# Kernel optimization log

Hardware: AMD Instinct MI355X
Metric: run time of the kernel (lower is better)

Reference implementation:

```python
import jax, jax.numpy as jnp
import numpy as np

# ---- static hyperparams (from comp_encoding.__init__ / DMPNNEncoderLayer) ----
B = 512            # number of molecules in the batch (wrapper's python loop)
A = 128            # padded atoms per molecule == max_mol_len
E = 256            # padded directed bonds per molecule
K = 6              # max incoming bonds gathered per bond/atom
ATOM_FDIM = 133
BOND_FDIM = 14
H = 128            # d_hidden = max_mol_len
DEPTH = 3
G = 2048           # global feature dim (Morgan fingerprint)


def _mol_lens():
    ml = np.array(jax.random.randint(jax.random.fold_in(jax.random.key(0), 5), (B,), 16, H + 1))
    ml[0] = H  # ensure comp_dim == max(mol_lens) == H so per-row padding is a no-op
    return ml


def setup_inputs() -> dict:
    key = jax.random.key(0)
    ks = jax.random.split(key, 10)
    atom_feature = jax.random.normal(ks[0], (B, A, ATOM_FDIM), jnp.float32)
    f_ini_atoms_bond = jax.random.normal(ks[1], (B, E, ATOM_FDIM + BOND_FDIM), jnp.float32)
    atom_to_incoming_bond = jax.random.randint(ks[2], (B, A, K), 0, E)
    mapping = jax.random.randint(ks[3], (B, E, K), 0, E)
    global_f = jax.random.normal(ks[4], (B, G), jnp.float32)
    mol_lens = _mol_lens()  # static numpy ints (constants, drive output shapes)
    W_i = jax.random.normal(ks[6], (H, ATOM_FDIM + BOND_FDIM), jnp.float32) / np.float32(np.sqrt(ATOM_FDIM + BOND_FDIM))
    W_h = jax.random.normal(ks[7], (H, H), jnp.float32) / np.float32(np.sqrt(H))
    W_o = jax.random.normal(ks[8], (H, ATOM_FDIM + H), jnp.float32) / np.float32(np.sqrt(ATOM_FDIM + H))
    b_o = jax.random.normal(ks[9], (H,), jnp.float32) * 0.01
    return dict(atom_feature=atom_feature, f_ini_atoms_bond=f_ini_atoms_bond,
                atom_to_incoming_bond=atom_to_incoming_bond, mapping=mapping,
                global_f=global_f, mol_lens=mol_lens,
                W_i=W_i, W_h=W_h, W_o=W_o, b_o=b_o)


def _gather_sum(msg, idx):
    # msg: [B, E, H]; idx: [B, N, K] -> sum over K incoming messages: [B, N, H]
    b, n, k = idx.shape
    g = jnp.take_along_axis(msg, idx.reshape(b, n * k)[..., None], axis=1)
    return g.reshape(b, n, k, -1).sum(axis=2)


def reference(atom_feature, f_ini_atoms_bond, atom_to_incoming_bond, mapping,
              global_f, mol_lens, W_i, W_h, W_o, b_o):
    # DMPNN: W_i on initial directed-bond features
    inp = jnp.einsum('bef,hf->beh', f_ini_atoms_bond, W_i)   # [B, E, H]
    msg = jax.nn.relu(inp)
    for _ in range(DEPTH - 1):
        agg = _gather_sum(msg, mapping)                      # [B, E, H]
        msg = jax.nn.relu(inp + jnp.einsum('beh,gh->beg', agg, W_h))
    m2a = _gather_sum(msg, atom_to_incoming_bond)            # [B, A, H]
    cat = jnp.concatenate([atom_feature, m2a], axis=-1)      # [B, A, 133+H]
    atoms_h = jax.nn.relu(jnp.einsum('bad,hd->bah', cat, W_o) + b_o)  # [B, A, H]

    # wrapper: take first mol_len atom encodings per molecule, stack, build mask
    ml = np.asarray(mol_lens)
    valid = np.arange(A)[None, :] < ml[:, None]              # [B, A] static
    b_idx, a_idx = np.nonzero(valid)
    comp = atoms_h[b_idx, a_idx]                             # [sum(mol_lens), H]
    c_mask = jnp.asarray(valid.astype(np.float32))           # [B, comp_dim]
    return comp, c_mask
```

## Files before the change

### kernel.cpp

```cpp
#include <hip/hip_runtime.h>
#include <hip/hip_bf16.h>

typedef unsigned int   uint;
typedef unsigned short ushort;
typedef short bf16x8 __attribute__((ext_vector_type(8)));
typedef float f32x4  __attribute__((ext_vector_type(4)));

constexpr int Bm   = 512;
constexpr int Aa   = 128;
constexpr int Ee   = 256;
constexpr int Kk   = 6;
constexpr int AFD  = 133;
constexpr int FD   = 147;
constexpr int Hh   = 128;
constexpr int CATD = 261;
constexpr int KWI  = 192;
constexpr int KWO  = 320;
constexpr int MST  = 136;

__device__ __forceinline__ ushort f2b(float f) {
    uint u = __float_as_uint(f);
    u += 0x7FFFu + ((u >> 16) & 1u);
    return (ushort)(u >> 16);
}
__device__ __forceinline__ uint cvt2(float x, float y) {
    float2 t2; t2.x = x; t2.y = y;
    __hip_bfloat162 t = __float22bfloat162_rn(t2);
    uint r; __builtin_memcpy(&r, &t, 4); return r;
}
__device__ __forceinline__ float2 b2f2(uint p) {
    float2 r;
    r.x = __uint_as_float(p << 16);
    r.y = __uint_as_float(p & 0xFFFF0000u);
    return r;
}

__device__ __forceinline__ bf16x8 gsum6(const ushort* src, const int* mr, int ko) {
    float2 s0 = {0.f, 0.f}, s1 = {0.f, 0.f}, s2 = {0.f, 0.f}, s3 = {0.f, 0.f};
#pragma unroll
    for (int k = 0; k < Kk; ++k) {
        uint4 m = *(const uint4*)&src[mr[k] + ko];
        float2 a = b2f2(m.x); s0.x += a.x; s0.y += a.y;
        float2 b = b2f2(m.y); s1.x += b.x; s1.y += b.y;
        float2 d = b2f2(m.z); s2.x += d.x; s2.y += d.y;
        float2 e = b2f2(m.w); s3.x += e.x; s3.y += e.y;
    }
    uint4 o;
    o.x = cvt2(s0.x, s0.y); o.y = cvt2(s1.x, s1.y);
    o.z = cvt2(s2.x, s2.y); o.w = cvt2(s3.x, s3.y);
    bf16x8 r;
    __builtin_memcpy(&r, &o, 16);
    return r;
}

__device__ __forceinline__ bf16x8 ld_frag_f32(const float* sp, int c0, int lim) {
    float v[8];
#pragma unroll
    for (int d = 0; d < 8; ++d) v[d] = (c0 + d < lim) ? sp[d] : 0.f;
    uint4 o;
    o.x = cvt2(v[0], v[1]); o.y = cvt2(v[2], v[3]);
    o.z = cvt2(v[4], v[5]); o.w = cvt2(v[6], v[7]);
    bf16x8 r;
    __builtin_memcpy(&r, &o, 16);
    return r;
}

__global__ __launch_bounds__(256) void k_prep_w(const float* __restrict__ Wi,
                                                const float* __restrict__ Wh,
                                                const float* __restrict__ Wo,
                                                ushort* __restrict__ Wi_b,
                                                ushort* __restrict__ Wh_b,
                                                ushort* __restrict__ Wo_b) {
    const int h = blockIdx.x, t = threadIdx.x;
    for (int c = t; c < KWI; c += 256)
        Wi_b[h * KWI + c] = f2b(c < FD ? Wi[h * FD + c] : 0.f);
    for (int c = t; c < Hh; c += 256)
        Wh_b[h * Hh + c] = f2b(Wh[h * Hh + c]);
    for (int c = t; c < KWO; c += 256) {
        float v = 0.f;
        if (c < AFD)       v = Wo[h * CATD + c];
        else if (c >= 192) v = Wo[h * CATD + AFD + (c - 192)];
        Wo_b[h * KWO + c] = f2b(v);
    }
}

__global__ __launch_bounds__(512) void k_scan(const int* __restrict__ ml,
                                              int* __restrict__ pfx) {
    __shared__ int s[512];
    int t = threadIdx.x;
    s[t] = ml[t];
    __syncthreads();
    for (int off = 1; off < 512; off <<= 1) {
        int v = (t >= off) ? s[t - off] : 0;
        __syncthreads();
        s[t] += v;
        __syncthreads();
    }
    pfx[t + 1] = s[t];
    if (t == 0) pfx[0] = 0;
}

__global__ __launch_bounds__(512, 2) void k_fused(
        const float* __restrict__ atomf,
        const float* __restrict__ fini,
        const int*   __restrict__ a2ib,
        const int*   __restrict__ mapping,
        const ushort* __restrict__ Wi_b,
        const ushort* __restrict__ Wh_b,
        const ushort* __restrict__ Wo_b,
        const float* __restrict__ bo,
        const int*   __restrict__ mol_lens,
        const int*   __restrict__ pfx,
        float* __restrict__ out,
        float* __restrict__ cmask) {
    __shared__ ushort msg[Ee * MST];
    __shared__ int    map_s[Ee * Kk];
    __shared__ int    a2_s[Aa * Kk];

    const int b    = blockIdx.x;
    const int tid  = threadIdx.x;
    const int wave = tid >> 6;
    const int lane = tid & 63;
    const int l15  = lane & 15, quad = lane >> 4;

    for (int i = tid; i < Ee * Kk; i += 512) map_s[i] = mapping[b * Ee * Kk + i];
    for (int i = tid; i < Aa * Kk; i += 512) a2_s[i]  = a2ib[b * Aa * Kk + i];
    const int len = mol_lens[b];
    if (tid < Aa) cmask[b * Aa + tid] = (tid < len) ? 1.0f : 0.0f;

    f32x4 acc[2][8];
#pragma unroll
    for (int i = 0; i < 2; ++i)
#pragma unroll
        for (int j = 0; j < 8; ++j) acc[i][j] = (f32x4){0.f, 0.f, 0.f, 0.f};

    const float* fsrc = fini + (size_t)b * Ee * FD;
#pragma unroll
    for (int c = 0; c < 3; ++c) {
#pragma unroll
        for (int ks = 0; ks < 2; ++ks) {
            const int c0 = c * 64 + ks * 32 + quad * 8;
            bf16x8 af[2];
#pragma unroll
            for (int i = 0; i < 2; ++i) {
                const int row = wave * 32 + i * 16 + l15;
                af[i] = ld_frag_f32(fsrc + (size_t)row * FD + c0, c0, FD);
            }
#pragma unroll
            for (int jh = 0; jh < 2; ++jh) {
                bf16x8 bf[4];
#pragma unroll
                for (int j = 0; j < 4; ++j)
                    bf[j] = *(const bf16x8*)&Wi_b[((jh * 4 + j) * 16 + l15) * KWI + c0];
#pragma unroll
                for (int i = 0; i < 2; ++i)
#pragma unroll
                    for (int j = 0; j < 4; ++j)
                        acc[i][jh * 4 + j] = __builtin_amdgcn_mfma_f32_16x16x32_bf16(
                            af[i], bf[j], acc[i][jh * 4 + j], 0, 0, 0);
            }
        }
    }

    uint2 inp_pk[2][8];
#pragma unroll
    for (int i = 0; i < 2; ++i)
#pragma unroll
        for (int j = 0; j < 8; ++j) {
            f32x4 a4 = acc[i][j];
            uint2 p;
            p.x = cvt2(a4[0], a4[1]);
            p.y = cvt2(a4[2], a4[3]);
            inp_pk[i][j] = p;
            int col = j * 16 + l15;
#pragma unroll
            for (int reg = 0; reg < 4; ++reg) {
                int row = wave * 32 + i * 16 + quad * 4 + reg;
                float v = a4[reg] > 0.f ? a4[reg] : 0.f;
                msg[row * MST + col] = f2b(v);
            }
        }
    __syncthreads();

    int mr[2][Kk];
#pragma unroll
    for (int i = 0; i < 2; ++i) {
        int row = wave * 32 + i * 16 + l15;
#pragma unroll
        for (int k = 0; k < Kk; ++k) mr[i][k] = map_s[row * Kk + k] * MST;
    }

#pragma unroll
    for (int h = 0; h < 2; ++h) {
#pragma unroll
        for (int i = 0; i < 2; ++i)
#pragma unroll
            for (int j = 0; j < 8; ++j) {
                float2 lo = b2f2(inp_pk[i][j].x);
                float2 hi = b2f2(inp_pk[i][j].y);
                acc[i][j] = (f32x4){lo.x, lo.y, hi.x, hi.y};
            }
#pragma unroll
        for (int ks = 0; ks < 4; ++ks) {
            const int ko = ks * 32 + quad * 8;
            bf16x8 af[2];
#pragma unroll
            for (int i = 0; i < 2; ++i) af[i] = gsum6(msg, mr[i], ko);
#pragma unroll
            for (int jh = 0; jh < 2; ++jh) {
                bf16x8 bf[4];
#pragma unroll
                for (int j = 0; j < 4; ++j)
                    bf[j] = *(const bf16x8*)&Wh_b[((jh * 4 + j) * 16 + l15) * Hh + ko];
#pragma unroll
                for (int i = 0; i < 2; ++i)
#pragma unroll
                    for (int j = 0; j < 4; ++j)
                        acc[i][jh * 4 + j] = __builtin_amdgcn_mfma_f32_16x16x32_bf16(
                            af[i], bf[j], acc[i][jh * 4 + j], 0, 0, 0);
            }
        }
        __syncthreads();
#pragma unroll
        for (int i = 0; i < 2; ++i)
#pragma unroll
            for (int j = 0; j < 8; ++j) {
                int col = j * 16 + l15;
#pragma unroll
                for (int reg = 0; reg < 4; ++reg) {
                    int row = wave * 32 + i * 16 + quad * 4 + reg;
                    float v = acc[i][j][reg];
                    msg[row * MST + col] = f2b(v > 0.f ? v : 0.f);
                }
            }
        __syncthreads();
    }

    f32x4 ro[8];
#pragma unroll
    for (int j = 0; j < 8; ++j) ro[j] = (f32x4){0.f, 0.f, 0.f, 0.f};

    {
        int ar[Kk];
        const int row = wave * 16 + l15;
#pragma unroll
        for (int k = 0; k < Kk; ++k) ar[k] = a2_s[row * Kk + k] * MST;
#pragma unroll
        for (int ks = 0; ks < 4; ++ks) {
            const int ko = ks * 32 + quad * 8;
            bf16x8 a0 = gsum6(msg, ar, ko);
#pragma unroll
            for (int jh = 0; jh < 2; ++jh) {
                bf16x8 bf[4];
#pragma unroll
                for (int j = 0; j < 4; ++j)
                    bf[j] = *(const bf16x8*)&Wo_b[((jh * 4 + j) * 16 + l15) * KWO + 192 + ko];
#pragma unroll
                for (int j = 0; j < 4; ++j)
                    ro[jh * 4 + j] = __builtin_amdgcn_mfma_f32_16x16x32_bf16(
                        a0, bf[j], ro[jh * 4 + j], 0, 0, 0);
            }
        }
    }

    const float* asrc = atomf + (size_t)b * Aa * AFD;
#pragma unroll
    for (int c = 0; c < 3; ++c) {
#pragma unroll
        for (int ks = 0; ks < 2; ++ks) {
            const int c0 = c * 64 + ks * 32 + quad * 8;
            const int row = wave * 16 + l15;
            bf16x8 a0 = ld_frag_f32(asrc + (size_t)row * AFD + c0, c0, AFD);
#pragma unroll
            for (int jh = 0; jh < 2; ++jh) {
                bf16x8 bf[4];
#pragma unroll
                for (int j = 0; j < 4; ++j)
                    bf[j] = *(const bf16x8*)&Wo_b[((jh * 4 + j) * 16 + l15) * KWO + c0];
#pragma unroll
                for (int j = 0; j < 4; ++j)
                    ro[jh * 4 + j] = __builtin_amdgcn_mfma_f32_16x16x32_bf16(
                        a0, bf[j], ro[jh * 4 + j], 0, 0, 0);
            }
        }
    }

    const int base = pfx[b];
#pragma unroll
    for (int j = 0; j < 8; ++j) {
        int col = j * 16 + l15;
        float bv = bo[col];
#pragma unroll
        for (int reg = 0; reg < 4; ++reg) {
            int a = wave * 16 + quad * 4 + reg;
            if (a < len) {
                float v = ro[j][reg] + bv;
                out[(size_t)(base + a) * Hh + col] = v > 0.f ? v : 0.f;
            }
        }
    }
}

extern "C" void kernel_launch(void* const* d_in, const int* in_sizes, int n_in,
                              void* d_out, int out_size, void* d_ws, size_t ws_size,
                              hipStream_t stream) {
    const float* atom_feature = (const float*)d_in[0];
    const float* f_ini        = (const float*)d_in[1];
    const int*   a2ib         = (const int*)d_in[2];
    const int*   mapping      = (const int*)d_in[3];
    const int*   mol_lens     = (const int*)d_in[5];
    const float* Wi           = (const float*)d_in[6];
    const float* Wh           = (const float*)d_in[7];
    const float* Wo           = (const float*)d_in[8];
    const float* bo           = (const float*)d_in[9];
    float* out = (float*)d_out;

    ushort* Wi_b = (ushort*)d_ws;
    ushort* Wh_b = Wi_b + 128 * KWI;
    ushort* Wo_b = Wh_b + 128 * Hh;
    int*    pfx  = (int*)(Wo_b + 128 * KWO);

    float* cmask = out + ((size_t)out_size - (size_t)Bm * Aa);

    k_prep_w<<<128, 256, 0, stream>>>(Wi, Wh, Wo, Wi_b, Wh_b, Wo_b);
    k_scan  <<<1, 512, 0, stream>>>(mol_lens, pfx);
    k_fused <<<Bm, 512, 0, stream>>>(atom_feature, f_ini, a2ib, mapping,
                                     Wi_b, Wh_b, Wo_b, bo, mol_lens, pfx,
                                     out, cmask);
}
```

Measured before the change: 274.6 us.

## Swizzle message LDS layout and load gather indices straight into registers

Replaces the padded message tile in shared memory (row stride 136) with an unpadded 128-wide layout that XOR-swizzles 8-element column groups by row, so both the scattered stores and the 16-byte gathers avoid bank conflicts. The mapping and atom-to-bond index tables no longer go through shared memory; each lane reads its own six indices from global memory into registers. This shrinks LDS use per block, which may allow more resident blocks, and drops a staging pass and a barrier dependency. The cost is extra XOR arithmetic on every message access and uncoalesced global index loads.

```diff
diff --git a/kernel.cpp b/kernel.cpp
--- a/kernel.cpp
+++ b/kernel.cpp
@@ -16,7 +16,10 @@
 constexpr int CATD = 261;
 constexpr int KWI  = 192;
 constexpr int KWO  = 320;
-constexpr int MST  = 136;
+
+__device__ __forceinline__ int msg_idx(int row, int col) {
+    return row * 128 + (col ^ ((row & 7) << 3));
+}
 
 __device__ __forceinline__ ushort f2b(float f) {
     uint u = __float_as_uint(f);
@@ -39,7 +42,8 @@
     float2 s0 = {0.f, 0.f}, s1 = {0.f, 0.f}, s2 = {0.f, 0.f}, s3 = {0.f, 0.f};
 #pragma unroll
     for (int k = 0; k < Kk; ++k) {
-        uint4 m = *(const uint4*)&src[mr[k] + ko];
+        const int sw = (mr[k] >> 4) & 56;
+        uint4 m = *(const uint4*)&src[mr[k] + (ko ^ sw)];
         float2 a = b2f2(m.x); s0.x += a.x; s0.y += a.y;
         float2 b = b2f2(m.y); s1.x += b.x; s1.y += b.y;
         float2 d = b2f2(m.z); s2.x += d.x; s2.y += d.y;
@@ -113,9 +117,7 @@
         const int*   __restrict__ pfx,
         float* __restrict__ out,
         float* __restrict__ cmask) {
-    __shared__ ushort msg[Ee * MST];
-    __shared__ int    map_s[Ee * Kk];
-    __shared__ int    a2_s[Aa * Kk];
+    __shared__ ushort msg[Ee * 128];
 
     const int b    = blockIdx.x;
     const int tid  = threadIdx.x;
@@ -123,10 +125,17 @@
     const int lane = tid & 63;
     const int l15  = lane & 15, quad = lane >> 4;
 
-    for (int i = tid; i < Ee * Kk; i += 512) map_s[i] = mapping[b * Ee * Kk + i];
-    for (int i = tid; i < Aa * Kk; i += 512) a2_s[i]  = a2ib[b * Aa * Kk + i];
     const int len = mol_lens[b];
     if (tid < Aa) cmask[b * Aa + tid] = (tid < len) ? 1.0f : 0.0f;
+
+    int mr[2][Kk];
+#pragma unroll
+    for (int i = 0; i < 2; ++i) {
+        const int row = wave * 32 + i * 16 + l15;
+        const int* mp = &mapping[((size_t)b * Ee + row) * Kk];
+#pragma unroll
+        for (int k = 0; k < Kk; ++k) mr[i][k] = mp[k] * 128;
+    }
 
     f32x4 acc[2][8];
 #pragma unroll
@@ -172,23 +181,15 @@
             p.x = cvt2(a4[0], a4[1]);
             p.y = cvt2(a4[2], a4[3]);
             inp_pk[i][j] = p;
-            int col = j * 16 + l15;
+            const int col = j * 16 + l15;
 #pragma unroll
             for (int reg = 0; reg < 4; ++reg) {
-                int row = wave * 32 + i * 16 + quad * 4 + reg;
+                const int row = wave * 32 + i * 16 + quad * 4 + reg;
                 float v = a4[reg] > 0.f ? a4[reg] : 0.f;
-                msg[row * MST + col] = f2b(v);
+                msg[msg_idx(row, col)] = f2b(v);
             }
         }
     __syncthreads();
-
-    int mr[2][Kk];
-#pragma unroll
-    for (int i = 0; i < 2; ++i) {
-        int row = wave * 32 + i * 16 + l15;
-#pragma unroll
-        for (int k = 0; k < Kk; ++k) mr[i][k] = map_s[row * Kk + k] * MST;
-    }
 
 #pragma unroll
     for (int h = 0; h < 2; ++h) {
@@ -225,12 +226,12 @@
         for (int i = 0; i < 2; ++i)
 #pragma unroll
             for (int j = 0; j < 8; ++j) {
-                int col = j * 16 + l15;
+                const int col = j * 16 + l15;
 #pragma unroll
                 for (int reg = 0; reg < 4; ++reg) {
-                    int row = wave * 32 + i * 16 + quad * 4 + reg;
+                    const int row = wave * 32 + i * 16 + quad * 4 + reg;
                     float v = acc[i][j][reg];
-                    msg[row * MST + col] = f2b(v > 0.f ? v : 0.f);
+                    msg[msg_idx(row, col)] = f2b(v > 0.f ? v : 0.f);
                 }
             }
         __syncthreads();
@@ -239,12 +240,14 @@
     f32x4 ro[8];
 #pragma unroll
     for (int j = 0; j < 8; ++j) ro[j] = (f32x4){0.f, 0.f, 0.f, 0.f};
+
+    const int arow = wave * 16 + l15;
 
     {
         int ar[Kk];
-        const int row = wave * 16 + l15;
-#pragma unroll
-        for (int k = 0; k < Kk; ++k) ar[k] = a2_s[row * Kk + k] * MST;
+        const int* ap = &a2ib[((size_t)b * Aa + arow) * Kk];
+#pragma unroll
+        for (int k = 0; k < Kk; ++k) ar[k] = ap[k] * 128;
 #pragma unroll
         for (int ks = 0; ks < 4; ++ks) {
             const int ko = ks * 32 + quad * 8;
@@ -269,8 +272,7 @@
 #pragma unroll
         for (int ks = 0; ks < 2; ++ks) {
             const int c0 = c * 64 + ks * 32 + quad * 8;
-            const int row = wave * 16 + l15;
-            bf16x8 a0 = ld_frag_f32(asrc + (size_t)row * AFD + c0, c0, AFD);
+            bf16x8 a0 = ld_frag_f32(asrc + (size_t)arow * AFD + c0, c0, AFD);
 #pragma unroll
             for (int jh = 0; jh < 2; ++jh) {
                 bf16x8 bf[4];
@@ -288,11 +290,11 @@
     const int base = pfx[b];
 #pragma unroll
     for (int j = 0; j < 8; ++j) {
-        int col = j * 16 + l15;
-        float bv = bo[col];
+        const int col = j * 16 + l15;
+        const float bv = bo[col];
 #pragma unroll
         for (int reg = 0; reg < 4; ++reg) {
-            int a = wave * 16 + quad * 4 + reg;
+            const int a = wave * 16 + quad * 4 + reg;
             if (a < len) {
                 float v = ro[j][reg] + bv;
                 out[(size_t)(base + a) * Hh + col] = v > 0.f ? v : 0.f;
```

Result: slower. 297.4 us (+8.3%).

## Stage bond and atom features into LDS as bf16 before MFMA GEMMs

Applied to the files above, without the earlier changes.

The kernel now copies each molecule's fp32 bond-feature and atom-feature rows into a padded bf16 shared-memory buffer with coalesced loads. Previously each lane did strided 8-float global reads and converted them per fragment. The atom-feature staging is placed inside the second message-passing iteration so its loads can overlap compute, and the K loop shrinks from 192 to 160 columns. The new ~78KB staging buffer roughly doubles LDS use per block, which likely drops residency from two blocks per CU to one.

```diff
diff --git a/kernel.cpp b/kernel.cpp
--- a/kernel.cpp
+++ b/kernel.cpp
@@ -17,6 +17,7 @@
 constexpr int KWI  = 192;
 constexpr int KWO  = 320;
 constexpr int MST  = 136;
+constexpr int FST  = 152;
 
 __device__ __forceinline__ ushort f2b(float f) {
     uint u = __float_as_uint(f);
@@ -48,18 +49,6 @@
     uint4 o;
     o.x = cvt2(s0.x, s0.y); o.y = cvt2(s1.x, s1.y);
     o.z = cvt2(s2.x, s2.y); o.w = cvt2(s3.x, s3.y);
-    bf16x8 r;
-    __builtin_memcpy(&r, &o, 16);
-    return r;
-}
-
-__device__ __forceinline__ bf16x8 ld_frag_f32(const float* sp, int c0, int lim) {
-    float v[8];
-#pragma unroll
-    for (int d = 0; d < 8; ++d) v[d] = (c0 + d < lim) ? sp[d] : 0.f;
-    uint4 o;
-    o.x = cvt2(v[0], v[1]); o.y = cvt2(v[2], v[3]);
-    o.z = cvt2(v[4], v[5]); o.w = cvt2(v[6], v[7]);
     bf16x8 r;
     __builtin_memcpy(&r, &o, 16);
     return r;
@@ -113,6 +102,7 @@
         const int*   __restrict__ pfx,
         float* __restrict__ out,
         float* __restrict__ cmask) {
+    __shared__ ushort stage_l[Ee * FST + 8];
     __shared__ ushort msg[Ee * MST];
     __shared__ int    map_s[Ee * Kk];
     __shared__ int    a2_s[Aa * Kk];
@@ -123,10 +113,19 @@
     const int lane = tid & 63;
     const int l15  = lane & 15, quad = lane >> 4;
 
+    const float* fsrc = fini + (size_t)b * Ee * FD;
+    for (int i = tid; i < Ee * FST; i += 512) {
+        int r = i / FST;
+        int c = i - r * FST;
+        float v = (c < FD) ? fsrc[r * FD + c] : 0.f;
+        stage_l[i] = f2b(v);
+    }
+    if (tid < 8) stage_l[Ee * FST + tid] = 0;
     for (int i = tid; i < Ee * Kk; i += 512) map_s[i] = mapping[b * Ee * Kk + i];
     for (int i = tid; i < Aa * Kk; i += 512) a2_s[i]  = a2ib[b * Aa * Kk + i];
     const int len = mol_lens[b];
     if (tid < Aa) cmask[b * Aa + tid] = (tid < len) ? 1.0f : 0.0f;
+    __syncthreads();
 
     f32x4 acc[2][8];
 #pragma unroll
@@ -134,31 +133,27 @@
 #pragma unroll
         for (int j = 0; j < 8; ++j) acc[i][j] = (f32x4){0.f, 0.f, 0.f, 0.f};
 
-    const float* fsrc = fini + (size_t)b * Ee * FD;
-#pragma unroll
-    for (int c = 0; c < 3; ++c) {
-#pragma unroll
-        for (int ks = 0; ks < 2; ++ks) {
-            const int c0 = c * 64 + ks * 32 + quad * 8;
-            bf16x8 af[2];
-#pragma unroll
-            for (int i = 0; i < 2; ++i) {
-                const int row = wave * 32 + i * 16 + l15;
-                af[i] = ld_frag_f32(fsrc + (size_t)row * FD + c0, c0, FD);
-            }
-#pragma unroll
-            for (int jh = 0; jh < 2; ++jh) {
-                bf16x8 bf[4];
+#pragma unroll
+    for (int ksi = 0; ksi < 5; ++ksi) {
+        const int c0 = ksi * 32 + quad * 8;
+        bf16x8 af[2];
+#pragma unroll
+        for (int i = 0; i < 2; ++i) {
+            const int row = wave * 32 + i * 16 + l15;
+            af[i] = *(const bf16x8*)&stage_l[row * FST + c0];
+        }
+#pragma unroll
+        for (int jh = 0; jh < 2; ++jh) {
+            bf16x8 bf[4];
+#pragma unroll
+            for (int j = 0; j < 4; ++j)
+                bf[j] = *(const bf16x8*)&Wi_b[((jh * 4 + j) * 16 + l15) * KWI + c0];
+#pragma unroll
+            for (int i = 0; i < 2; ++i)
 #pragma unroll
                 for (int j = 0; j < 4; ++j)
-                    bf[j] = *(const bf16x8*)&Wi_b[((jh * 4 + j) * 16 + l15) * KWI + c0];
-#pragma unroll
-                for (int i = 0; i < 2; ++i)
-#pragma unroll
-                    for (int j = 0; j < 4; ++j)
-                        acc[i][jh * 4 + j] = __builtin_amdgcn_mfma_f32_16x16x32_bf16(
-                            af[i], bf[j], acc[i][jh * 4 + j], 0, 0, 0);
-            }
+                    acc[i][jh * 4 + j] = __builtin_amdgcn_mfma_f32_16x16x32_bf16(
+                        af[i], bf[j], acc[i][jh * 4 + j], 0, 0, 0);
         }
     }
 
@@ -172,10 +167,10 @@
             p.x = cvt2(a4[0], a4[1]);
             p.y = cvt2(a4[2], a4[3]);
             inp_pk[i][j] = p;
-            int col = j * 16 + l15;
+            const int col = j * 16 + l15;
 #pragma unroll
             for (int reg = 0; reg < 4; ++reg) {
-                int row = wave * 32 + i * 16 + quad * 4 + reg;
+                const int row = wave * 32 + i * 16 + quad * 4 + reg;
                 float v = a4[reg] > 0.f ? a4[reg] : 0.f;
                 msg[row * MST + col] = f2b(v);
             }
@@ -185,13 +180,22 @@
     int mr[2][Kk];
 #pragma unroll
     for (int i = 0; i < 2; ++i) {
-        int row = wave * 32 + i * 16 + l15;
+        const int row = wave * 32 + i * 16 + l15;
 #pragma unroll
         for (int k = 0; k < Kk; ++k) mr[i][k] = map_s[row * Kk + k] * MST;
     }
 
 #pragma unroll
     for (int h = 0; h < 2; ++h) {
+        if (h == 1) {
+            const float* asrc = atomf + (size_t)b * Aa * AFD;
+            for (int i = tid; i < Aa * FST; i += 512) {
+                int r = i / FST;
+                int c = i - r * FST;
+                float v = (c < AFD) ? asrc[r * AFD + c] : 0.f;
+                stage_l[i] = f2b(v);
+            }
+        }
 #pragma unroll
         for (int i = 0; i < 2; ++i)
 #pragma unroll
@@ -225,10 +229,10 @@
         for (int i = 0; i < 2; ++i)
 #pragma unroll
             for (int j = 0; j < 8; ++j) {
-                int col = j * 16 + l15;
+                const int col = j * 16 + l15;
 #pragma unroll
                 for (int reg = 0; reg < 4; ++reg) {
-                    int row = wave * 32 + i * 16 + quad * 4 + reg;
+                    const int row = wave * 32 + i * 16 + quad * 4 + reg;
                     float v = acc[i][j][reg];
                     msg[row * MST + col] = f2b(v > 0.f ? v : 0.f);
                 }
@@ -240,11 +244,12 @@
 #pragma unroll
     for (int j = 0; j < 8; ++j) ro[j] = (f32x4){0.f, 0.f, 0.f, 0.f};
 
+    const int arow = wave * 16 + l15;
+
     {
         int ar[Kk];
-        const int row = wave * 16 + l15;
-#pragma unroll
-        for (int k = 0; k < Kk; ++k) ar[k] = a2_s[row * Kk + k] * MST;
+#pragma unroll
+        for (int k = 0; k < Kk; ++k) ar[k] = a2_s[arow * Kk + k] * MST;
 #pragma unroll
         for (int ks = 0; ks < 4; ++ks) {
             const int ko = ks * 32 + quad * 8;
@@ -263,36 +268,31 @@
         }
     }
 
-    const float* asrc = atomf + (size_t)b * Aa * AFD;
-#pragma unroll
-    for (int c = 0; c < 3; ++c) {
-#pragma unroll
-        for (int ks = 0; ks < 2; ++ks) {
-            const int c0 = c * 64 + ks * 32 + quad * 8;
-            const int row = wave * 16 + l15;
-            bf16x8 a0 = ld_frag_f32(asrc + (size_t)row * AFD + c0, c0, AFD);
-#pragma unroll
-            for (int jh = 0; jh < 2; ++jh) {
-                bf16x8 bf[4];
-#pragma unroll
-                for (int j = 0; j < 4; ++j)
-                    bf[j] = *(const bf16x8*)&Wo_b[((jh * 4 + j) * 16 + l15) * KWO + c0];
-#pragma unroll
-                for (int j = 0; j < 4; ++j)
-                    ro[jh * 4 + j] = __builtin_amdgcn_mfma_f32_16x16x32_bf16(
-                        a0, bf[j], ro[jh * 4 + j], 0, 0, 0);
-            }
+#pragma unroll
+    for (int ksi = 0; ksi < 5; ++ksi) {
+        const int c0 = ksi * 32 + quad * 8;
+        bf16x8 a0 = *(const bf16x8*)&stage_l[arow * FST + c0];
+#pragma unroll
+        for (int jh = 0; jh < 2; ++jh) {
+            bf16x8 bf[4];
+#pragma unroll
+            for (int j = 0; j < 4; ++j)
+                bf[j] = *(const bf16x8*)&Wo_b[((jh * 4 + j) * 16 + l15) * KWO + c0];
+#pragma unroll
+            for (int j = 0; j < 4; ++j)
+                ro[jh * 4 + j] = __builtin_amdgcn_mfma_f32_16x16x32_bf16(
+                    a0, bf[j], ro[jh * 4 + j], 0, 0, 0);
         }
     }
 
     const int base = pfx[b];
 #pragma unroll
     for (int j = 0; j < 8; ++j) {
-        int col = j * 16 + l15;
-        float bv = bo[col];
+        const int col = j * 16 + l15;
+        const float bv = bo[col];
 #pragma unroll
         for (int reg = 0; reg < 4; ++reg) {
-            int a = wave * 16 + quad * 4 + reg;
+            const int a = wave * 16 + quad * 4 + reg;
             if (a < len) {
                 float v = ro[j][reg] + bv;
                 out[(size_t)(base + a) * Hh + col] = v > 0.f ? v : 0.f;
```

After: 354.8 us. 1.29x slower.
